# Performance work log

Hardware: AMD Instinct MI355X
Metric: run time of the kernel (lower is better)

The kernel has to match this reference:

```python
import jax, jax.numpy as jnp
import numpy as np

N = 10000       # nodes
E = 160000      # edges (avg degree 16)
WIDTH = 256
SCALE = 2
HID = WIDTH * SCALE   # 512
HEAD_DIM = 64
EW = WIDTH // 2       # edge embed width = 128
BOND = (5, 6, 2, 17)
RES = 1.0


def _lin(key, fan_in, fan_out):
    kw, kb = jax.random.split(key)
    s = 1.0 / np.sqrt(fan_in)
    W = jax.random.uniform(kw, (fan_in, fan_out), minval=-s, maxval=s, dtype=jnp.float32)
    b = jax.random.uniform(kb, (fan_out,), minval=-s, maxval=s, dtype=jnp.float32)
    return W, b


def setup_inputs() -> dict:
    key = jax.random.key(0)
    ks = jax.random.split(key, 24)
    inp = {}
    inp['x'] = jax.random.normal(ks[0], (N, WIDTH), dtype=jnp.float32)
    inp['edge_index'] = jax.random.randint(ks[1], (2, E), 0, N, dtype=jnp.int32)
    inp['edge_attr'] = jax.random.randint(ks[2], (E, 4), 0, 3, dtype=jnp.int32)
    inp['edge_embed'] = jax.random.normal(ks[3], (E, EW), dtype=jnp.float32)
    # EmbedBlock tables: size[i]+1 rows; tables 1..3 have padding_idx=0 (row 0 zeroed)
    inp['emb0'] = jax.random.normal(ks[4], (BOND[0] + 1, EW), dtype=jnp.float32)
    for i, k in zip((1, 2, 3), (ks[5], ks[6], ks[7])):
        t = jax.random.normal(k, (BOND[i] + 1, EW), dtype=jnp.float32)
        inp[f'emb{i}'] = t.at[0].set(0.0)
    # learned log-scales (torch inits to zeros; use small values so paths are non-trivial)
    inp['init0_e'] = 0.1 * jax.random.normal(ks[8], (4,), dtype=jnp.float32)
    inp['init0'] = 0.1 * jax.random.normal(ks[9], (4,), dtype=jnp.float32)  # hop*2+2 = 4
    inp['W_pre'], inp['b_pre'] = _lin(ks[10], WIDTH, WIDTH)
    inp['W_msg0'], inp['b_msg0'] = _lin(ks[11], WIDTH, HID)
    inp['W_q'], inp['b_q'] = _lin(ks[12], WIDTH, HID)
    inp['W_k'], inp['b_k'] = _lin(ks[13], WIDTH, HID)
    inp['W_v'], inp['b_v'] = _lin(ks[14], WIDTH, HID)
    inp['W_r0'], inp['b_r0'] = _lin(ks[15], EW, HID)
    inp['W_r1'], inp['b_r1'] = _lin(ks[16], EW, HID)
    inp['W_r2'], inp['b_r2'] = _lin(ks[17], EW, HID)
    inp['W_post'], inp['b_post'] = _lin(ks[18], HID, WIDTH)
    return inp


def _ln(h):
    m = h.mean(-1, keepdims=True)
    v = ((h - m) ** 2).mean(-1, keepdims=True)
    return (h - m) / jnp.sqrt(v + 1e-5)


def _gelu(h):
    return jax.nn.gelu(h, approximate=False)  # torch nn.GELU default (erf)


def reference(x, edge_index, edge_attr, edge_embed,
              emb0, emb1, emb2, emb3, init0_e, init0,
              W_pre, b_pre, W_msg0, b_msg0, W_q, b_q, W_k, b_k, W_v, b_v,
              W_r0, b_r0, W_r1, b_r1, W_r2, b_r2, W_post, b_post):
    # pre: Linear + LayerNorm(no affine)
    xx = _ln(x @ W_pre + b_pre)                                  # [N, W]
    # EmbedBlock(bond_size): weighted sum of 4 embeddings, then average with x_ema
    xw = jnp.exp(init0_e) / jnp.sqrt(jnp.sum(jnp.exp(init0_e)))
    ee = (emb0[edge_attr[:, 0]] * xw[0] + emb1[edge_attr[:, 1]] * xw[1]
          + emb2[edge_attr[:, 2]] * xw[2] + emb3[edge_attr[:, 3]] * xw[3])  # [E, EW]
    ee = (ee + edge_embed) / 2
    # message: gather endpoints (source_to_target: row0=j source, row1=i target)
    src, dst = edge_index[0], edge_index[1]
    x_i = xx[dst]                                                # [E, W]
    x_j = xx[src]                                                # [E, W]
    s_e = jnp.exp(init0[-2])
    s_v = jnp.exp(init0[-1])
    x_q = x_i @ W_q + b_q + (ee @ W_r0 + b_r0) * s_e             # [E, HID]
    x_k = x_j @ W_k + b_k + (ee @ W_r1 + b_r1) * s_e
    x_v = _gelu(x_j @ W_v + b_v + (ee @ W_r2 + b_r2) * s_v)
    # inline per-edge multi-head dot-product attention
    att = jnp.sum((x_q * x_k).reshape(E, -1, HEAD_DIM), axis=-1, keepdims=True) / np.sqrt(HEAD_DIM)
    att = jnp.exp(att * init0[0] + init0[1])                     # [E, H, 1]
    msg = (x_v.reshape(E, -1, HEAD_DIM) * att).reshape(E, HID)
    # scatter-add aggregation at targets
    agg = jax.ops.segment_sum(msg, dst, num_segments=N)          # [N, HID]
    xx2 = _gelu(xx @ W_msg0 + b_msg0) + agg
    out = x + (xx2 @ W_post + b_post) * RES                      # [N, W]
    return out
```

## Files before the change

kernel.cpp:

```cpp
#include <hip/hip_runtime.h>
#include <hip/hip_bf16.h>
#include <math.h>

#define NN   10000
#define EE   160000
#define WID  256
#define HIDD 512
#define EWID 128

typedef __attribute__((ext_vector_type(8))) short bf16x8;
typedef __attribute__((ext_vector_type(4))) float f32x4;

__device__ __forceinline__ float geluf(float x) {
    return 0.5f * x * (1.0f + erff(x * 0.70710678118654752f));
}

__device__ __forceinline__ unsigned short f2bf(float f) {
    unsigned int u = __float_as_uint(f);
    u += 0x7fffu + ((u >> 16) & 1u);
    return (unsigned short)(u >> 16);
}

__device__ __forceinline__ float bfup(unsigned int u, int hi) {
    return hi ? __uint_as_float(u & 0xffff0000u) : __uint_as_float(u << 16);
}

__global__ __launch_bounds__(256) void k_cvt(const float* __restrict__ W0,
                                             const float* __restrict__ W1,
                                             const float* __restrict__ W2,
                                             unsigned short* __restrict__ out) {
    int tid = blockIdx.x * 256 + threadIdx.x;
    int p = tid >> 16;
    int rem = tid & 65535;
    int n = rem >> 7, k = rem & 127;
    const float* W = p == 0 ? W0 : p == 1 ? W1 : W2;
    out[tid] = f2bf(W[k * HIDD + n]);
}

__global__ __launch_bounds__(256) void k_cvtn(const float* __restrict__ W0,
                                              const float* __restrict__ W1,
                                              const float* __restrict__ W2,
                                              const float* __restrict__ W3,
                                              unsigned short* __restrict__ out) {
    int tid = blockIdx.x * 256 + threadIdx.x;
    int sel = tid >> 17;
    int rem = tid & 131071;
    int n = rem >> 8, k = rem & 255;
    const float* W = sel == 0 ? W0 : sel == 1 ? W1 : sel == 2 ? W2 : W3;
    out[tid] = f2bf(W[k * HIDD + n]);
}

__global__ __launch_bounds__(256) void k_cvt2(const float* __restrict__ Wpre,
                                              const float* __restrict__ Wpost,
                                              unsigned short* __restrict__ WpreT,
                                              unsigned short* __restrict__ WpostT) {
    int tid = blockIdx.x * 256 + threadIdx.x;
    if (tid < 65536) {
        int n = tid >> 8, k = tid & 255;
        WpreT[tid] = f2bf(Wpre[k * WID + n]);
    } else {
        int rem = tid - 65536;
        int n = rem >> 9, k = rem & 511;
        WpostT[rem] = f2bf(Wpost[k * WID + n]);
    }
}

__global__ __launch_bounds__(256) void k_ee(
    const int* __restrict__ eattr, const float* __restrict__ eemb,
    const float* __restrict__ emb0, const float* __restrict__ emb1,
    const float* __restrict__ emb2, const float* __restrict__ emb3,
    const float* __restrict__ i0e,
    unsigned short* __restrict__ eeF) {
    int c = blockIdx.x * 256 + threadIdx.x;
    int lane6 = c & 63;
    int kb = (c >> 6) & 3;
    int tile = c >> 8;
    int edge = tile * 16 + (lane6 & 15);
    int k0 = kb * 32 + (lane6 >> 4) * 8;
    float ev0 = __expf(i0e[0]), ev1 = __expf(i0e[1]),
          ev2 = __expf(i0e[2]), ev3 = __expf(i0e[3]);
    float rsum = rsqrtf(ev0 + ev1 + ev2 + ev3);
    float xw0 = ev0 * rsum, xw1 = ev1 * rsum, xw2 = ev2 * rsum, xw3 = ev3 * rsum;
    int4 at = *(const int4*)&eattr[edge * 4];
    float t0[8], t1[8], t2[8], t3[8], te[8];
    *(float4*)&t0[0] = *(const float4*)&emb0[at.x * EWID + k0];
    *(float4*)&t0[4] = *(const float4*)&emb0[at.x * EWID + k0 + 4];
    *(float4*)&t1[0] = *(const float4*)&emb1[at.y * EWID + k0];
    *(float4*)&t1[4] = *(const float4*)&emb1[at.y * EWID + k0 + 4];
    *(float4*)&t2[0] = *(const float4*)&emb2[at.z * EWID + k0];
    *(float4*)&t2[4] = *(const float4*)&emb2[at.z * EWID + k0 + 4];
    *(float4*)&t3[0] = *(const float4*)&emb3[at.w * EWID + k0];
    *(float4*)&t3[4] = *(const float4*)&emb3[at.w * EWID + k0 + 4];
    *(float4*)&te[0] = *(const float4*)&eemb[edge * EWID + k0];
    *(float4*)&te[4] = *(const float4*)&eemb[edge * EWID + k0 + 4];
    bf16x8 p;
    #pragma unroll
    for (int j = 0; j < 8; ++j)
        p[j] = (short)f2bf(0.5f * (xw0 * t0[j] + xw1 * t1[j] + xw2 * t2[j]
                                   + xw3 * t3[j] + te[j]));
    *(bf16x8*)&eeF[c * 8] = p;
}

__global__ __launch_bounds__(256, 4) void k_pre(const float* __restrict__ x,
                                                const unsigned short* __restrict__ WpreT,
                                                const float* __restrict__ bp,
                                                unsigned short* __restrict__ xxb) {
    __shared__ __align__(16) float ot[16 * 260];
    int t = threadIdx.x;
    int lane = t & 63, w = t >> 6;
    int l15 = lane & 15, quad = lane >> 4;
    int r0 = blockIdx.x * 16;
    bf16x8 af[8];
    #pragma unroll
    for (int kb = 0; kb < 8; ++kb) {
        int k0 = kb * 32 + quad * 8;
        float a8[8];
        *(float4*)&a8[0] = *(const float4*)&x[(r0 + l15) * WID + k0];
        *(float4*)&a8[4] = *(const float4*)&x[(r0 + l15) * WID + k0 + 4];
        bf16x8 p;
        #pragma unroll
        for (int j = 0; j < 8; ++j) p[j] = (short)f2bf(a8[j]);
        af[kb] = p;
    }
    #pragma unroll
    for (int tb = 0; tb < 4; ++tb) {
        int c = w * 64 + tb * 16 + l15;
        float bias = bp[c];
        f32x4 acc = {bias, bias, bias, bias};
        #pragma unroll
        for (int kb = 0; kb < 8; ++kb) {
            bf16x8 bfr = *(const bf16x8*)&WpreT[c * WID + kb * 32 + quad * 8];
            acc = __builtin_amdgcn_mfma_f32_16x16x32_bf16(af[kb], bfr, acc, 0, 0, 0);
        }
        #pragma unroll
        for (int r = 0; r < 4; ++r)
            ot[(quad * 4 + r) * 260 + c] = acc[r];
    }
    __syncthreads();
    #pragma unroll
    for (int rr = 0; rr < 4; ++rr) {
        int row = w * 4 + rr;
        float s = 0.f, s2 = 0.f;
        #pragma unroll
        for (int k2 = 0; k2 < 4; ++k2) {
            float v = ot[row * 260 + lane + 64 * k2];
            s += v; s2 += v * v;
        }
        #pragma unroll
        for (int off = 32; off >= 1; off >>= 1) {
            s  += __shfl_xor(s,  off, 64);
            s2 += __shfl_xor(s2, off, 64);
        }
        float m = s * (1.f / WID);
        float rstd = rsqrtf(s2 * (1.f / WID) - m * m + 1e-5f);
        #pragma unroll
        for (int k2 = 0; k2 < 4; ++k2) {
            int c = lane + 64 * k2;
            xxb[(r0 + row) * WID + c] = f2bf((ot[row * 260 + c] - m) * rstd);
        }
    }
}

__global__ __launch_bounds__(256, 4) void k_qkvm(
    const unsigned short* __restrict__ xxb,
    const unsigned short* __restrict__ WTn,
    const float* __restrict__ bq, const float* __restrict__ bk,
    const float* __restrict__ bv, const float* __restrict__ bm,
    unsigned short* __restrict__ XQp, unsigned short* __restrict__ XKp,
    unsigned short* __restrict__ XVp, float* __restrict__ AG) {
    int t = threadIdx.x;
    int r0 = blockIdx.x * 32;
    int sel = blockIdx.y;
    const float* bsel = sel == 0 ? bq : sel == 1 ? bk : sel == 2 ? bv : bm;
    const unsigned short* Wp = WTn + sel * (HIDD * WID);
    unsigned short* outp = sel == 0 ? XQp : sel == 1 ? XKp : XVp;
    int lane = t & 63, w = t >> 6;
    int l15 = lane & 15, quad = lane >> 4;
    int rA = min(r0 + l15, NN - 1);
    int rB = min(r0 + 16 + l15, NN - 1);
    bf16x8 af0[8], af1[8];
    #pragma unroll
    for (int kb = 0; kb < 8; ++kb) {
        af0[kb] = *(const bf16x8*)&xxb[rA * WID + kb * 32 + quad * 8];
        af1[kb] = *(const bf16x8*)&xxb[rB * WID + kb * 32 + quad * 8];
    }
    #pragma unroll
    for (int tb = 0; tb < 8; ++tb) {
        int c = w * 128 + tb * 16;
        float bias = bsel[c + l15];
        f32x4 acc0 = {bias, bias, bias, bias};
        f32x4 acc1 = {bias, bias, bias, bias};
        #pragma unroll
        for (int kb = 0; kb < 8; ++kb) {
            bf16x8 bfr = *(const bf16x8*)&Wp[(c + l15) * WID + kb * 32 + quad * 8];
            acc0 = __builtin_amdgcn_mfma_f32_16x16x32_bf16(af0[kb], bfr, acc0, 0, 0, 0);
            acc1 = __builtin_amdgcn_mfma_f32_16x16x32_bf16(af1[kb], bfr, acc1, 0, 0, 0);
        }
        if (sel < 3) {
            int base = ((w * 64 + (tb >> 1) * 16 + l15) << 1) + (tb & 1);
            #pragma unroll
            for (int r = 0; r < 4; ++r) {
                int n0 = r0 + quad * 4 + r;
                int n1 = n0 + 16;
                if (n0 < NN) outp[n0 * 512 + base] = f2bf(acc0[r]);
                if (n1 < NN) outp[n1 * 512 + base] = f2bf(acc1[r]);
            }
        } else {
            #pragma unroll
            for (int r = 0; r < 4; ++r) {
                int n0 = r0 + quad * 4 + r;
                int n1 = n0 + 16;
                if (n0 < NN) AG[n0 * HIDD + c + l15] = geluf(acc0[r]);
                if (n1 < NN) AG[n1 * HIDD + c + l15] = geluf(acc1[r]);
            }
        }
    }
}

__global__ __launch_bounds__(256, 4) void k_edge(
    const int* __restrict__ eidx,
    const unsigned short* __restrict__ eeF,
    const float* __restrict__ i0,
    const unsigned int* __restrict__ XQp, const unsigned int* __restrict__ XKp,
    const unsigned int* __restrict__ XVp,
    const unsigned short* __restrict__ WrT,
    const float* __restrict__ br0, const float* __restrict__ br1,
    const float* __restrict__ br2,
    float* __restrict__ agg) {
    __shared__ __align__(16) unsigned short Bs[2048 * 8];
    int t = threadIdx.x;
    int lane = t & 63, w = t >> 6;
    int l15 = lane & 15, quad = lane >> 4;
    int cg = blockIdx.x;
    int tile = blockIdx.y * 4 + w;
    int e0 = tile * 16;

    float a_sc = i0[0], a_bi = i0[1];
    float s_e = expf(i0[2]), s_v = expf(i0[3]);
    float c_sc = 0.125f * a_sc;

    bf16x8 af[4];
    #pragma unroll
    for (int kb = 0; kb < 4; ++kb)
        af[kb] = *(const bf16x8*)&eeF[((tile * 4 + kb) * 64 + lane) * 8];

    int ndp[4], nsp[4], nda[4];
    #pragma unroll
    for (int r = 0; r < 4; ++r) {
        int en = e0 + quad * 4 + r;
        int sn = eidx[en], dn = eidx[EE + en];
        ndp[r] = dn * 256 + cg * 64 + l15;
        nsp[r] = sn * 256 + cg * 64 + l15;
        nda[r] = dn * HIDD + cg * 128 + l15;
    }

    unsigned int pq[4][4], pk[4][4];
    #pragma unroll
    for (int a = 0; a < 4; ++a)
        #pragma unroll
        for (int r = 0; r < 4; ++r) {
            pq[a][r] = XQp[ndp[r] + a * 16];
            pk[a][r] = XKp[nsp[r] + a * 16];
        }

    const bf16x8* ssrc0 = (const bf16x8*)&WrT[(cg * 128 + l15) * 128 + w * 32 + quad * 8];
    bf16x8* sdst0 = (bf16x8*)&Bs[(w * 64 + lane) * 8];

    #pragma unroll
    for (int i = 0; i < 8; ++i) sdst0[i * 256] = ssrc0[i * 16 * 16];
    __syncthreads();
    float q[8][4];
    #pragma unroll
    for (int tb = 0; tb < 8; ++tb) {
        float bias = br0[cg * 128 + tb * 16 + l15];
        f32x4 acc = {bias, bias, bias, bias};
        #pragma unroll
        for (int kb = 0; kb < 4; ++kb) {
            bf16x8 bfr = *(const bf16x8*)&Bs[(tb * 256 + kb * 64 + lane) * 8];
            acc = __builtin_amdgcn_mfma_f32_16x16x32_bf16(af[kb], bfr, acc, 0, 0, 0);
        }
        #pragma unroll
        for (int r = 0; r < 4; ++r)
            q[tb][r] = bfup(pq[tb >> 1][r], tb & 1) + s_e * acc[r];
    }
    unsigned int pv[4][4];
    #pragma unroll
    for (int a = 0; a < 4; ++a)
        #pragma unroll
        for (int r = 0; r < 4; ++r) pv[a][r] = XVp[nsp[r] + a * 16];
    __syncthreads();

    #pragma unroll
    for (int i = 0; i < 8; ++i) sdst0[i * 256] = ssrc0[8192 + i * 256];
    __syncthreads();
    float d0[4] = {0.f, 0.f, 0.f, 0.f}, d1[4] = {0.f, 0.f, 0.f, 0.f};
    #pragma unroll
    for (int tb = 0; tb < 8; ++tb) {
        float bias = br1[cg * 128 + tb * 16 + l15];
        f32x4 acc = {bias, bias, bias, bias};
        #pragma unroll
        for (int kb = 0; kb < 4; ++kb) {
            bf16x8 bfr = *(const bf16x8*)&Bs[(tb * 256 + kb * 64 + lane) * 8];
            acc = __builtin_amdgcn_mfma_f32_16x16x32_bf16(af[kb], bfr, acc, 0, 0, 0);
        }
        #pragma unroll
        for (int r = 0; r < 4; ++r) {
            float kv = bfup(pk[tb >> 1][r], tb & 1) + s_e * acc[r];
            float pp = q[tb][r] * kv;
            if (tb < 4) d0[r] += pp; else d1[r] += pp;
        }
    }
    float att0[4], att1[4];
    #pragma unroll
    for (int off = 8; off >= 1; off >>= 1) {
        #pragma unroll
        for (int r = 0; r < 4; ++r) {
            d0[r] += __shfl_xor(d0[r], off, 64);
            d1[r] += __shfl_xor(d1[r], off, 64);
        }
    }
    #pragma unroll
    for (int r = 0; r < 4; ++r) {
        att0[r] = expf(d0[r] * c_sc + a_bi);
        att1[r] = expf(d1[r] * c_sc + a_bi);
    }
    __syncthreads();

    #pragma unroll
    for (int i = 0; i < 8; ++i) sdst0[i * 256] = ssrc0[16384 + i * 256];
    __syncthreads();
    #pragma unroll
    for (int tb = 0; tb < 8; ++tb) {
        float bias = br2[cg * 128 + tb * 16 + l15];
        f32x4 acc = {bias, bias, bias, bias};
        #pragma unroll
        for (int kb = 0; kb < 4; ++kb) {
            bf16x8 bfr = *(const bf16x8*)&Bs[(tb * 256 + kb * 64 + lane) * 8];
            acc = __builtin_amdgcn_mfma_f32_16x16x32_bf16(af[kb], bfr, acc, 0, 0, 0);
        }
        #pragma unroll
        for (int r = 0; r < 4; ++r) {
            float v = geluf(bfup(pv[tb >> 1][r], tb & 1) + s_v * acc[r]);
            float m = v * (tb < 4 ? att0[r] : att1[r]);
            atomicAdd(&agg[nda[r] + tb * 16], m);
        }
    }
}

__global__ __launch_bounds__(256, 4) void k_post(const float* __restrict__ x,
    const float* __restrict__ agg,
    const unsigned short* __restrict__ WpT,
    const float* __restrict__ bp,
    float* __restrict__ out) {
    int t = threadIdx.x;
    int lane = t & 63, w = t >> 6;
    int l15 = lane & 15, quad = lane >> 4;
    int r0 = blockIdx.x * 16;
    bf16x8 af[16];
    #pragma unroll
    for (int kb = 0; kb < 16; ++kb) {
        int k0 = kb * 32 + quad * 8;
        float a8[8];
        *(float4*)&a8[0] = *(const float4*)&agg[(r0 + l15) * HIDD + k0];
        *(float4*)&a8[4] = *(const float4*)&agg[(r0 + l15) * HIDD + k0 + 4];
        bf16x8 p;
        #pragma unroll
        for (int j = 0; j < 8; ++j) p[j] = (short)f2bf(a8[j]);
        af[kb] = p;
    }
    #pragma unroll
    for (int tb = 0; tb < 4; ++tb) {
        int c = w * 64 + tb * 16 + l15;
        float bias = bp[c];
        f32x4 acc = {bias, bias, bias, bias};
        #pragma unroll
        for (int kb = 0; kb < 16; ++kb) {
            bf16x8 bfr = *(const bf16x8*)&WpT[c * HIDD + kb * 32 + quad * 8];
            acc = __builtin_amdgcn_mfma_f32_16x16x32_bf16(af[kb], bfr, acc, 0, 0, 0);
        }
        #pragma unroll
        for (int r = 0; r < 4; ++r) {
            int row = r0 + quad * 4 + r;
            out[row * WID + c] = x[row * WID + c] + acc[r];
        }
    }
}

extern "C" void kernel_launch(void* const* d_in, const int* in_sizes, int n_in,
                              void* d_out, int out_size, void* d_ws, size_t ws_size,
                              hipStream_t stream) {
    const float* x     = (const float*)d_in[0];
    const int*   eidx  = (const int*)  d_in[1];
    const int*   eattr = (const int*)  d_in[2];
    const float* eemb  = (const float*)d_in[3];
    const float* emb0  = (const float*)d_in[4];
    const float* emb1  = (const float*)d_in[5];
    const float* emb2  = (const float*)d_in[6];
    const float* emb3  = (const float*)d_in[7];
    const float* i0e   = (const float*)d_in[8];
    const float* i0    = (const float*)d_in[9];
    const float* Wpre  = (const float*)d_in[10];
    const float* bpre  = (const float*)d_in[11];
    const float* Wm    = (const float*)d_in[12];
    const float* bm    = (const float*)d_in[13];
    const float* Wq    = (const float*)d_in[14];
    const float* bq    = (const float*)d_in[15];
    const float* Wk    = (const float*)d_in[16];
    const float* bk    = (const float*)d_in[17];
    const float* Wv    = (const float*)d_in[18];
    const float* bv    = (const float*)d_in[19];
    const float* Wr0   = (const float*)d_in[20];
    const float* br0   = (const float*)d_in[21];
    const float* Wr1   = (const float*)d_in[22];
    const float* br1   = (const float*)d_in[23];
    const float* Wr2   = (const float*)d_in[24];
    const float* br2   = (const float*)d_in[25];
    const float* Wpost = (const float*)d_in[26];
    const float* bpost = (const float*)d_in[27];

    float* ws  = (float*)d_ws;
    float* agg = ws;
    unsigned short* xxb    = (unsigned short*)(ws + 5120000);
    unsigned short* XQp    = (unsigned short*)(ws + 6400000);
    unsigned short* XKp    = (unsigned short*)(ws + 8960000);
    unsigned short* XVp    = (unsigned short*)(ws + 11520000);
    unsigned short* WrT    = (unsigned short*)(ws + 14080000);
    unsigned short* WTn    = (unsigned short*)(ws + 14178304);
    unsigned short* WpreT  = (unsigned short*)(ws + 14440448);
    unsigned short* WpostT = (unsigned short*)(ws + 14473216);
    unsigned short* eeF    = (unsigned short*)(ws + 14538752);

    k_cvt<<<768, 256, 0, stream>>>(Wr0, Wr1, Wr2, WrT);
    k_cvtn<<<2048, 256, 0, stream>>>(Wq, Wk, Wv, Wm, WTn);
    k_cvt2<<<768, 256, 0, stream>>>(Wpre, Wpost, WpreT, WpostT);
    k_ee<<<10000, 256, 0, stream>>>(eattr, eemb, emb0, emb1, emb2, emb3, i0e, eeF);
    k_pre<<<625, 256, 0, stream>>>(x, WpreT, bpre, xxb);
    k_qkvm<<<dim3(313, 4), 256, 0, stream>>>(xxb, WTn, bq, bk, bv, bm,
                                             XQp, XKp, XVp, agg);
    k_edge<<<dim3(4, 2500), 256, 0, stream>>>(eidx, eeF, i0,
                                              (const unsigned int*)XQp,
                                              (const unsigned int*)XKp,
                                              (const unsigned int*)XVp,
                                              WrT, br0, br1, br2, agg);
    k_post<<<625, 256, 0, stream>>>(x, agg, WpostT, bpost, (float*)d_out);
}
```

Before: 694.0 us.

## Split edge kernel columns into one head per block and merge weight conversions

The edge attention kernel now handles 64 hidden columns (one head) per block instead of 128, doubling the column-group grid to 8. This halves the shared-memory tile, the per-thread gathered registers and the attention accumulators, and raises launch bounds to 6 blocks per SM for higher occupancy. In exchange, the edge indices, the edge-embedding fragments and the per-edge gathers are loaded twice as often. The three weight-conversion kernels are also merged into one launch to cut launch overhead.

```diff
diff --git a/kernel.cpp b/kernel.cpp
--- a/kernel.cpp
+++ b/kernel.cpp
@@ -25,43 +25,34 @@
     return hi ? __uint_as_float(u & 0xffff0000u) : __uint_as_float(u << 16);
 }
 
-__global__ __launch_bounds__(256) void k_cvt(const float* __restrict__ W0,
-                                             const float* __restrict__ W1,
-                                             const float* __restrict__ W2,
-                                             unsigned short* __restrict__ out) {
+__global__ __launch_bounds__(256) void k_cvtall(
+    const float* __restrict__ Wr0, const float* __restrict__ Wr1,
+    const float* __restrict__ Wr2,
+    const float* __restrict__ Wq, const float* __restrict__ Wk,
+    const float* __restrict__ Wv, const float* __restrict__ Wm,
+    const float* __restrict__ Wpre, const float* __restrict__ Wpost,
+    unsigned short* __restrict__ WrT, unsigned short* __restrict__ WTn,
+    unsigned short* __restrict__ WpreT, unsigned short* __restrict__ WpostT) {
     int tid = blockIdx.x * 256 + threadIdx.x;
-    int p = tid >> 16;
-    int rem = tid & 65535;
-    int n = rem >> 7, k = rem & 127;
-    const float* W = p == 0 ? W0 : p == 1 ? W1 : W2;
-    out[tid] = f2bf(W[k * HIDD + n]);
-}
-
-__global__ __launch_bounds__(256) void k_cvtn(const float* __restrict__ W0,
-                                              const float* __restrict__ W1,
-                                              const float* __restrict__ W2,
-                                              const float* __restrict__ W3,
-                                              unsigned short* __restrict__ out) {
-    int tid = blockIdx.x * 256 + threadIdx.x;
-    int sel = tid >> 17;
-    int rem = tid & 131071;
-    int n = rem >> 8, k = rem & 255;
-    const float* W = sel == 0 ? W0 : sel == 1 ? W1 : sel == 2 ? W2 : W3;
-    out[tid] = f2bf(W[k * HIDD + n]);
-}
-
-__global__ __launch_bounds__(256) void k_cvt2(const float* __restrict__ Wpre,
-                                              const float* __restrict__ Wpost,
-                                              unsigned short* __restrict__ WpreT,
-                                              unsigned short* __restrict__ WpostT) {
-    int tid = blockIdx.x * 256 + threadIdx.x;
-    if (tid < 65536) {
-        int n = tid >> 8, k = tid & 255;
-        WpreT[tid] = f2bf(Wpre[k * WID + n]);
+    if (tid < 196608) {
+        int p = tid >> 16, rem = tid & 65535;
+        int n = rem >> 7, k = rem & 127;
+        const float* W = p == 0 ? Wr0 : p == 1 ? Wr1 : Wr2;
+        WrT[tid] = f2bf(W[k * HIDD + n]);
+    } else if (tid < 720896) {
+        int u = tid - 196608;
+        int sel = u >> 17, rem = u & 131071;
+        int n = rem >> 8, k = rem & 255;
+        const float* W = sel == 0 ? Wq : sel == 1 ? Wk : sel == 2 ? Wv : Wm;
+        WTn[u] = f2bf(W[k * HIDD + n]);
+    } else if (tid < 786432) {
+        int u = tid - 720896;
+        int n = u >> 8, k = u & 255;
+        WpreT[u] = f2bf(Wpre[k * WID + n]);
     } else {
-        int rem = tid - 65536;
-        int n = rem >> 9, k = rem & 511;
-        WpostT[rem] = f2bf(Wpost[k * WID + n]);
+        int u = tid - 786432;
+        int n = u >> 9, k = u & 511;
+        WpostT[u] = f2bf(Wpost[k * WID + n]);
     }
 }
 
@@ -217,7 +208,7 @@
     }
 }
 
-__global__ __launch_bounds__(256, 4) void k_edge(
+__global__ __launch_bounds__(256, 6) void k_edge(
     const int* __restrict__ eidx,
     const unsigned short* __restrict__ eeF,
     const float* __restrict__ i0,
@@ -227,7 +218,7 @@
     const float* __restrict__ br0, const float* __restrict__ br1,
     const float* __restrict__ br2,
     float* __restrict__ agg) {
-    __shared__ __align__(16) unsigned short Bs[2048 * 8];
+    __shared__ __align__(16) unsigned short Bs[1024 * 8];
     int t = threadIdx.x;
     int lane = t & 63, w = t >> 6;
     int l15 = lane & 15, quad = lane >> 4;
@@ -244,105 +235,95 @@
     for (int kb = 0; kb < 4; ++kb)
         af[kb] = *(const bf16x8*)&eeF[((tile * 4 + kb) * 64 + lane) * 8];
 
-    int ndp[4], nsp[4], nda[4];
+    int dn[4], sn[4];
     #pragma unroll
     for (int r = 0; r < 4; ++r) {
         int en = e0 + quad * 4 + r;
-        int sn = eidx[en], dn = eidx[EE + en];
-        ndp[r] = dn * 256 + cg * 64 + l15;
-        nsp[r] = sn * 256 + cg * 64 + l15;
-        nda[r] = dn * HIDD + cg * 128 + l15;
-    }
-
-    unsigned int pq[4][4], pk[4][4];
-    #pragma unroll
-    for (int a = 0; a < 4; ++a)
+        sn[r] = eidx[en];
+        dn[r] = eidx[EE + en];
+    }
+
+    unsigned int pq[2][4], pk[2][4];
+    #pragma unroll
+    for (int a = 0; a < 2; ++a)
         #pragma unroll
         for (int r = 0; r < 4; ++r) {
-            pq[a][r] = XQp[ndp[r] + a * 16];
-            pk[a][r] = XKp[nsp[r] + a * 16];
-        }
-
-    const bf16x8* ssrc0 = (const bf16x8*)&WrT[(cg * 128 + l15) * 128 + w * 32 + quad * 8];
-    bf16x8* sdst0 = (bf16x8*)&Bs[(w * 64 + lane) * 8];
-
-    #pragma unroll
-    for (int i = 0; i < 8; ++i) sdst0[i * 256] = ssrc0[i * 16 * 16];
-    __syncthreads();
-    float q[8][4];
-    #pragma unroll
-    for (int tb = 0; tb < 8; ++tb) {
-        float bias = br0[cg * 128 + tb * 16 + l15];
+            pq[a][r] = XQp[dn[r] * 256 + cg * 32 + l15 + a * 16];
+            pk[a][r] = XKp[sn[r] * 256 + cg * 32 + l15 + a * 16];
+        }
+
+    int s_off = (cg * 64 + l15) * 128 + w * 32 + quad * 8;
+    bf16x8* sdst = (bf16x8*)Bs + t;
+    const bf16x8* bsr = (const bf16x8*)Bs;
+
+    #pragma unroll
+    for (int i = 0; i < 4; ++i)
+        sdst[i * 256] = *(const bf16x8*)&WrT[s_off + i * 2048];
+    __syncthreads();
+    float q[4][4];
+    #pragma unroll
+    for (int tb = 0; tb < 4; ++tb) {
+        float bias = br0[cg * 64 + tb * 16 + l15];
         f32x4 acc = {bias, bias, bias, bias};
         #pragma unroll
-        for (int kb = 0; kb < 4; ++kb) {
-            bf16x8 bfr = *(const bf16x8*)&Bs[(tb * 256 + kb * 64 + lane) * 8];
-            acc = __builtin_amdgcn_mfma_f32_16x16x32_bf16(af[kb], bfr, acc, 0, 0, 0);
-        }
+        for (int kb = 0; kb < 4; ++kb)
+            acc = __builtin_amdgcn_mfma_f32_16x16x32_bf16(af[kb], bsr[tb * 256 + kb * 64 + lane], acc, 0, 0, 0);
         #pragma unroll
         for (int r = 0; r < 4; ++r)
             q[tb][r] = bfup(pq[tb >> 1][r], tb & 1) + s_e * acc[r];
     }
-    unsigned int pv[4][4];
-    #pragma unroll
-    for (int a = 0; a < 4; ++a)
-        #pragma unroll
-        for (int r = 0; r < 4; ++r) pv[a][r] = XVp[nsp[r] + a * 16];
-    __syncthreads();
-
-    #pragma unroll
-    for (int i = 0; i < 8; ++i) sdst0[i * 256] = ssrc0[8192 + i * 256];
-    __syncthreads();
-    float d0[4] = {0.f, 0.f, 0.f, 0.f}, d1[4] = {0.f, 0.f, 0.f, 0.f};
-    #pragma unroll
-    for (int tb = 0; tb < 8; ++tb) {
-        float bias = br1[cg * 128 + tb * 16 + l15];
+    unsigned int pv[2][4];
+    #pragma unroll
+    for (int a = 0; a < 2; ++a)
+        #pragma unroll
+        for (int r = 0; r < 4; ++r)
+            pv[a][r] = XVp[sn[r] * 256 + cg * 32 + l15 + a * 16];
+    __syncthreads();
+
+    #pragma unroll
+    for (int i = 0; i < 4; ++i)
+        sdst[i * 256] = *(const bf16x8*)&WrT[65536 + s_off + i * 2048];
+    __syncthreads();
+    float d[4] = {0.f, 0.f, 0.f, 0.f};
+    #pragma unroll
+    for (int tb = 0; tb < 4; ++tb) {
+        float bias = br1[cg * 64 + tb * 16 + l15];
         f32x4 acc = {bias, bias, bias, bias};
         #pragma unroll
-        for (int kb = 0; kb < 4; ++kb) {
-            bf16x8 bfr = *(const bf16x8*)&Bs[(tb * 256 + kb * 64 + lane) * 8];
-            acc = __builtin_amdgcn_mfma_f32_16x16x32_bf16(af[kb], bfr, acc, 0, 0, 0);
-        }
+        for (int kb = 0; kb < 4; ++kb)
+            acc = __builtin_amdgcn_mfma_f32_16x16x32_bf16(af[kb], bsr[tb * 256 + kb * 64 + lane], acc, 0, 0, 0);
         #pragma unroll
         for (int r = 0; r < 4; ++r) {
             float kv = bfup(pk[tb >> 1][r], tb & 1) + s_e * acc[r];
-            float pp = q[tb][r] * kv;
-            if (tb < 4) d0[r] += pp; else d1[r] += pp;
-        }
-    }
-    float att0[4], att1[4];
-    #pragma unroll
-    for (int off = 8; off >= 1; off >>= 1) {
-        #pragma unroll
-        for (int r = 0; r < 4; ++r) {
-            d0[r] += __shfl_xor(d0[r], off, 64);
-            d1[r] += __shfl_xor(d1[r], off, 64);
-        }
-    }
-    #pragma unroll
-    for (int r = 0; r < 4; ++r) {
-        att0[r] = expf(d0[r] * c_sc + a_bi);
-        att1[r] = expf(d1[r] * c_sc + a_bi);
-    }
-    __syncthreads();
-
-    #pragma unroll
-    for (int i = 0; i < 8; ++i) sdst0[i * 256] = ssrc0[16384 + i * 256];
-    __syncthreads();
-    #pragma unroll
-    for (int tb = 0; tb < 8; ++tb) {
-        float bias = br2[cg * 128 + tb * 16 + l15];
+            d[r] += q[tb][r] * kv;
+        }
+    }
+    float att[4];
+    #pragma unroll
+    for (int off = 8; off >= 1; off >>= 1)
+        #pragma unroll
+        for (int r = 0; r < 4; ++r)
+            d[r] += __shfl_xor(d[r], off, 64);
+    #pragma unroll
+    for (int r = 0; r < 4; ++r)
+        att[r] = expf(d[r] * c_sc + a_bi);
+    __syncthreads();
+
+    #pragma unroll
+    for (int i = 0; i < 4; ++i)
+        sdst[i * 256] = *(const bf16x8*)&WrT[131072 + s_off + i * 2048];
+    __syncthreads();
+    #pragma unroll
+    for (int tb = 0; tb < 4; ++tb) {
+        float bias = br2[cg * 64 + tb * 16 + l15];
         f32x4 acc = {bias, bias, bias, bias};
         #pragma unroll
-        for (int kb = 0; kb < 4; ++kb) {
-            bf16x8 bfr = *(const bf16x8*)&Bs[(tb * 256 + kb * 64 + lane) * 8];
-            acc = __builtin_amdgcn_mfma_f32_16x16x32_bf16(af[kb], bfr, acc, 0, 0, 0);
-        }
+        for (int kb = 0; kb < 4; ++kb)
+            acc = __builtin_amdgcn_mfma_f32_16x16x32_bf16(af[kb], bsr[tb * 256 + kb * 64 + lane], acc, 0, 0, 0);
         #pragma unroll
         for (int r = 0; r < 4; ++r) {
             float v = geluf(bfup(pv[tb >> 1][r], tb & 1) + s_v * acc[r]);
-            float m = v * (tb < 4 ? att0[r] : att1[r]);
-            atomicAdd(&agg[nda[r] + tb * 16], m);
+            atomicAdd(&agg[dn[r] * HIDD + cg * 64 + tb * 16 + l15], v * att[r]);
         }
     }
 }
@@ -430,14 +411,13 @@
     unsigned short* WpostT = (unsigned short*)(ws + 14473216);
     unsigned short* eeF    = (unsigned short*)(ws + 14538752);
 
-    k_cvt<<<768, 256, 0, stream>>>(Wr0, Wr1, Wr2, WrT);
-    k_cvtn<<<2048, 256, 0, stream>>>(Wq, Wk, Wv, Wm, WTn);
-    k_cvt2<<<768, 256, 0, stream>>>(Wpre, Wpost, WpreT, WpostT);
+    k_cvtall<<<3584, 256, 0, stream>>>(Wr0, Wr1, Wr2, Wq, Wk, Wv, Wm, Wpre, Wpost,
+                                       WrT, WTn, WpreT, WpostT);
     k_ee<<<10000, 256, 0, stream>>>(eattr, eemb, emb0, emb1, emb2, emb3, i0e, eeF);
     k_pre<<<625, 256, 0, stream>>>(x, WpreT, bpre, xxb);
     k_qkvm<<<dim3(313, 4), 256, 0, stream>>>(xxb, WTn, bq, bk, bv, bm,
                                              XQp, XKp, XVp, agg);
-    k_edge<<<dim3(4, 2500), 256, 0, stream>>>(eidx, eeF, i0,
+    k_edge<<<dim3(8, 2500), 256, 0, stream>>>(eidx, eeF, i0,
                                               (const unsigned int*)XQp,
                                               (const unsigned int*)XKp,
                                               (const unsigned int*)XVp,
```

New measurement: 655.5 us. 5.6% less time.
